# Optimization experiments

Hardware: AMD Instinct MI355X
Metric: run time of the kernel (lower is better)

## Reference

```python
import jax, jax.numpy as jnp
import numpy as np

CHEB_K = 3  # from init_kwargs


def setup_inputs() -> dict:
    key = jax.random.key(0)
    k1, k2, k3, k4 = jax.random.split(key, 4)
    B, N, C_IN, C_OUT, D = 32, 4096, 32, 64, 16
    x = jax.random.normal(k1, (B, N, C_IN), dtype=jnp.float32)
    node_embeddings = jax.random.normal(k2, (N, D), dtype=jnp.float32)
    laplacian_mx = jnp.zeros((N, N), dtype=jnp.float32)  # unused by forward
    weights_pool = jax.random.normal(k3, (D, CHEB_K, C_IN, C_OUT), dtype=jnp.float32) * 0.1
    bias_pool = jax.random.normal(k4, (D, C_OUT), dtype=jnp.float32) * 0.1
    return {
        'x': x,
        'node_embeddings': node_embeddings,
        'laplacian_mx': laplacian_mx,
        'weights_pool': weights_pool,
        'bias_pool': bias_pool,
    }


def reference(x, node_embeddings, laplacian_mx, weights_pool, bias_pool):
    N = node_embeddings.shape[0]
    # adaptive adjacency: softmax(relu(E E^T)) over rows
    supports = jax.nn.softmax(jax.nn.relu(node_embeddings @ node_embeddings.T), axis=1)
    # Chebyshev recursion T_0=I, T_1=A, T_k = 2A T_{k-1} - T_{k-2}
    support_set = [jnp.eye(N, dtype=x.dtype), supports]
    for _ in range(2, CHEB_K):
        support_set.append(2.0 * supports @ support_set[-1] - support_set[-2])
    supports_k = jnp.stack(support_set, axis=0)  # [K, N, N]
    # per-node generated weights/bias
    weights = jnp.einsum('nd,dkio->nkio', node_embeddings, weights_pool)  # [N,K,I,O]
    bias = node_embeddings @ bias_pool  # [N, O]
    # graph propagation: [K,N,N] x [B,N,I] -> [B,K,N,I] -> [B,N,K,I]
    x_g = jnp.einsum('knm,bmc->bknc', supports_k, x).transpose(0, 2, 1, 3)
    # per-node grouped GEMM
    out = jnp.einsum('bnki,nkio->bno', x_g, weights) + bias
    return out
```

## Files before the change

### kernel.cpp

```cpp
#include <hip/hip_runtime.h>
#include <hip/hip_bf16.h>

#define N_NODES 4096
#define BATCH   32
#define CIN     32
#define COUT    64
#define DEMB    16
#define NCOL    (BATCH * CIN)
#define KIO     (3 * CIN * COUT)
#define SPLITK  2

typedef __bf16 bf16x8 __attribute__((ext_vector_type(8)));
typedef float  floatx4 __attribute__((ext_vector_type(4)));

__device__ inline void load_lds16(const void* g, void* l) {
    __builtin_amdgcn_global_load_lds(
        (const __attribute__((address_space(1))) void*)g,
        (__attribute__((address_space(3))) void*)l, 16, 0, 0);
}

__global__ __launch_bounds__(256) void compute_U_kernel(
        const float* __restrict__ E, __hip_bfloat16* __restrict__ U,
        float* __restrict__ invRow) {
    const int n0   = blockIdx.x * 8;
    const int t    = threadIdx.x;
    const int lane = t & 63, wave = t >> 6;
    __shared__ float red[4][8];

    float en[8][DEMB];
#pragma unroll
    for (int r = 0; r < 8; ++r) {
        const float4* er = (const float4*)&E[(size_t)(n0 + r) * DEMB];
        const float4 a0 = er[0], a1 = er[1], a2 = er[2], a3 = er[3];
        en[r][ 0]=a0.x; en[r][ 1]=a0.y; en[r][ 2]=a0.z; en[r][ 3]=a0.w;
        en[r][ 4]=a1.x; en[r][ 5]=a1.y; en[r][ 6]=a1.z; en[r][ 7]=a1.w;
        en[r][ 8]=a2.x; en[r][ 9]=a2.y; en[r][10]=a2.z; en[r][11]=a2.w;
        en[r][12]=a3.x; en[r][13]=a3.y; en[r][14]=a3.z; en[r][15]=a3.w;
    }

    float sum[8] = {0.f, 0.f, 0.f, 0.f, 0.f, 0.f, 0.f, 0.f};

    for (int tile = 0; tile < 16; ++tile) {
        const int c = tile * 256 + t;
        const float4* em4 = (const float4*)&E[(size_t)c * DEMB];
        const float4 b0 = em4[0], b1 = em4[1], b2 = em4[2], b3 = em4[3];
        float em[DEMB];
        em[ 0]=b0.x; em[ 1]=b0.y; em[ 2]=b0.z; em[ 3]=b0.w;
        em[ 4]=b1.x; em[ 5]=b1.y; em[ 6]=b1.z; em[ 7]=b1.w;
        em[ 8]=b2.x; em[ 9]=b2.y; em[10]=b2.z; em[11]=b2.w;
        em[12]=b3.x; em[13]=b3.y; em[14]=b3.z; em[15]=b3.w;
#pragma unroll
        for (int r = 0; r < 8; ++r) {
            float dt = 0.f;
#pragma unroll
            for (int d = 0; d < DEMB; ++d) dt += en[r][d] * em[d];
            const float ev = __expf(fmaxf(dt, 0.f));
            sum[r] += ev;
            U[(size_t)(n0 + r) * N_NODES + c] = __float2bfloat16(ev);
        }
    }
#pragma unroll
    for (int r = 0; r < 8; ++r)
#pragma unroll
        for (int off = 32; off > 0; off >>= 1) sum[r] += __shfl_xor(sum[r], off);
    if (lane == 0)
#pragma unroll
        for (int r = 0; r < 8; ++r) red[wave][r] = sum[r];
    __syncthreads();
    if (t < 8)
        invRow[n0 + t] = 1.0f / (red[0][t] + red[1][t] + red[2][t] + red[3][t]);
}

__global__ __launch_bounds__(256) void transpose_kernel(
        const float* __restrict__ x,
        __hip_bfloat16* __restrict__ Xt, __hip_bfloat16* __restrict__ Bt) {
    const int m0 = blockIdx.x * 64;
    const int b  = blockIdx.y;
    const int t  = threadIdx.x;
    __shared__ float tile[64][33];
    {
        const int ml = t >> 2, cg = (t & 3) * 8;
        const float* src = &x[((size_t)b * N_NODES + (m0 + ml)) * CIN + cg];
        const float4 r0 = *(const float4*)src;
        const float4 r1 = *(const float4*)(src + 4);
        tile[ml][cg+0] = r0.x; tile[ml][cg+1] = r0.y; tile[ml][cg+2] = r0.z; tile[ml][cg+3] = r0.w;
        tile[ml][cg+4] = r1.x; tile[ml][cg+5] = r1.y; tile[ml][cg+6] = r1.z; tile[ml][cg+7] = r1.w;
    }
    __syncthreads();
    {
        const int ml = t >> 2, cg = (t & 3) * 8;
        __hip_bfloat16* dst = &Xt[(size_t)(m0 + ml) * NCOL + b * CIN + cg];
#pragma unroll
        for (int j = 0; j < 8; ++j) dst[j] = __float2bfloat16(tile[ml][cg + j]);
    }
    {
        const int c = t >> 3, mg = (t & 7) * 8;
        __hip_bfloat16* dst = &Bt[(size_t)(b * CIN + c) * N_NODES + m0 + mg];
#pragma unroll
        for (int j = 0; j < 8; ++j) dst[j] = __float2bfloat16(tile[mg + j][c]);
    }
}

__global__ __launch_bounds__(256) void gen_w_kernel(
        const float* __restrict__ E, const float* __restrict__ Wp,
        __hip_bfloat16* __restrict__ Wn) {
    const int c   = blockIdx.x >> 3;
    const int oo0 = (blockIdx.x & 7) * 8;
    const int nc  = blockIdx.y * 64;
    const int t   = threadIdx.x;
    const int kk  = t & 31;
    const int oo  = oo0 + (t >> 5);

    __shared__ float et[64][DEMB];
    ((float4*)et)[t] = ((const float4*)&E[(size_t)nc * DEMB])[t];
    __syncthreads();

    const int srccol = (c * 32 + kk) * 64 + oo;
    float w[DEMB];
#pragma unroll
    for (int d = 0; d < DEMB; ++d) w[d] = Wp[(size_t)d * KIO + srccol];

    const int dstoff = c * 2048 + (oo >> 4) * 512 + (oo & 15) * 32 + kk;
    for (int nl = 0; nl < 64; ++nl) {
        float acc = 0.0f;
#pragma unroll
        for (int d = 0; d < DEMB; ++d) acc += et[nl][d] * w[d];
        Wn[(size_t)(nc + nl) * KIO + dstoff] = __float2bfloat16(acc);
    }
}

#define GBM 256
#define GBN 128
#define GBK 64
#define NBUF 3

__global__ __launch_bounds__(512, 2) void gemm_splitk_kernel(
        const __hip_bfloat16* __restrict__ A,
        const __hip_bfloat16* __restrict__ Bt,
        __hip_bfloat16* __restrict__ P,
        int M, int NC, int K) {
    const int t    = threadIdx.x;
    const int row0 = blockIdx.x * GBM;
    const int col0 = blockIdx.y * GBN;
    const int z    = blockIdx.z;
    const int NT   = (K >> 6) / SPLITK;
    const int kb0  = z * NT * GBK;

    __shared__ alignas(16) __hip_bfloat16 As[NBUF][GBM * GBK];
    __shared__ alignas(16) __hip_bfloat16 Bs[NBUF][GBN * GBK];

    const int lane = t & 63, wave = t >> 6;
    const int l16 = lane & 15, quad = lane >> 4;
    const int wr = wave >> 1, wc = wave & 1;
    const int wrow = wr * 64, wcol = wc * 64;
    const int xr = l16 & 7;

    auto stageA = [&](int buf, int kb, int s) {
        const int gi = s * 512 + t;
        const int r  = gi >> 3;
        const int cg = (gi & 7) ^ (r & 7);
        load_lds16(&A[(size_t)(row0 + r) * K + kb + cg * 8], &As[buf][gi * 8]);
    };
    auto stageB = [&](int buf, int kb, int s) {
        const int gi = s * 512 + t;
        const int r  = gi >> 3;
        const int cg = (gi & 7) ^ (r & 7);
        load_lds16(&Bt[(size_t)(col0 + r) * K + kb + cg * 8], &Bs[buf][gi * 8]);
    };

    floatx4 acc[4][4] = {};

#pragma unroll
    for (int s = 0; s < 4; ++s) stageA(0, kb0, s);
#pragma unroll
    for (int s = 0; s < 2; ++s) stageB(0, kb0, s);
#pragma unroll
    for (int s = 0; s < 4; ++s) stageA(1, kb0 + GBK, s);
#pragma unroll
    for (int s = 0; s < 2; ++s) stageB(1, kb0 + GBK, s);
    asm volatile("s_waitcnt vmcnt(6)" ::: "memory");
    __builtin_amdgcn_s_barrier();
    __builtin_amdgcn_sched_barrier(0);

    int cur = 0;
    for (int tt = 0; tt < NT; ++tt) {
        const int  nb  = (cur + 2 >= NBUF) ? cur + 2 - NBUF : cur + 2;
        const int  kbn = kb0 + (tt + 2) * GBK;
        const bool pf  = (tt + 2 < NT);

        bf16x8 af0[4], bf0[4];
#pragma unroll
        for (int i = 0; i < 4; ++i)
            af0[i] = *(const bf16x8*)&As[cur][(wrow + i * 16 + l16) * GBK +
                                             ((quad ^ xr) * 8)];
#pragma unroll
        for (int j = 0; j < 4; ++j)
            bf0[j] = *(const bf16x8*)&Bs[cur][(wcol + j * 16 + l16) * GBK +
                                             ((quad ^ xr) * 8)];
        if (pf) { stageA(nb, kbn, 0); stageA(nb, kbn, 1); stageB(nb, kbn, 0); }
        __builtin_amdgcn_s_barrier();
        __builtin_amdgcn_s_setprio(1);
#pragma unroll
        for (int i = 0; i < 4; ++i)
#pragma unroll
            for (int j = 0; j < 4; ++j)
                acc[i][j] = __builtin_amdgcn_mfma_f32_16x16x32_bf16(
                                af0[i], bf0[j], acc[i][j], 0, 0, 0);
        __builtin_amdgcn_s_setprio(0);
        __builtin_amdgcn_s_barrier();

        bf16x8 af1[4], bf1[4];
#pragma unroll
        for (int i = 0; i < 4; ++i)
            af1[i] = *(const bf16x8*)&As[cur][(wrow + i * 16 + l16) * GBK +
                                             (((4 + quad) ^ xr) * 8)];
#pragma unroll
        for (int j = 0; j < 4; ++j)
            bf1[j] = *(const bf16x8*)&Bs[cur][(wcol + j * 16 + l16) * GBK +
                                             (((4 + quad) ^ xr) * 8)];
        if (pf) { stageA(nb, kbn, 2); stageA(nb, kbn, 3); stageB(nb, kbn, 1); }
        __builtin_amdgcn_s_barrier();
        __builtin_amdgcn_s_setprio(1);
#pragma unroll
        for (int i = 0; i < 4; ++i)
#pragma unroll
            for (int j = 0; j < 4; ++j)
                acc[i][j] = __builtin_amdgcn_mfma_f32_16x16x32_bf16(
                                af1[i], bf1[j], acc[i][j], 0, 0, 0);
        __builtin_amdgcn_s_setprio(0);
        if (pf) asm volatile("s_waitcnt vmcnt(6)" ::: "memory");
        else    asm volatile("s_waitcnt vmcnt(0)" ::: "memory");
        __builtin_amdgcn_s_barrier();
        __builtin_amdgcn_sched_barrier(0);

        cur = (cur + 1 == NBUF) ? 0 : cur + 1;
    }

    __hip_bfloat16* Pz = P + (size_t)z * M * NC;
#pragma unroll
    for (int i = 0; i < 4; ++i)
#pragma unroll
        for (int j = 0; j < 4; ++j)
#pragma unroll
            for (int r = 0; r < 4; ++r) {
                const int rg = row0 + wrow + i * 16 + quad * 4 + r;
                const int cg = col0 + wcol + j * 16 + l16;
                Pz[(size_t)rg * NC + cg] = __float2bfloat16(acc[i][j][r]);
            }
}

__global__ __launch_bounds__(256) void combine1_kernel(
        const __hip_bfloat16* __restrict__ P, const float* __restrict__ invRow,
        __hip_bfloat16* __restrict__ Y, __hip_bfloat16* __restrict__ Yt,
        int M, int NC) {
    const int c0 = blockIdx.x * 64, m0 = blockIdx.y * 64;
    const int t = threadIdx.x;
    __shared__ float tile[64][65];
    const size_t stride = (size_t)M * NC;
#pragma unroll
    for (int j = 0; j < 16; ++j) {
        const int lin = t + j * 256;
        const int r = lin >> 6, c = lin & 63;
        const size_t idx = (size_t)(m0 + r) * NC + c0 + c;
        float s = 0.f;
#pragma unroll
        for (int z = 0; z < SPLITK; ++z) s += __bfloat162float(P[idx + z * stride]);
        s *= invRow[m0 + r];
        tile[r][c] = s;
        Y[idx] = __float2bfloat16(s);
    }
    __syncthreads();
#pragma unroll
    for (int j = 0; j < 16; ++j) {
        const int lin = t + j * 256;
        const int c = lin >> 6, r = lin & 63;
        Yt[(size_t)(c0 + c) * M + m0 + r] = __float2bfloat16(tile[r][c]);
    }
}

__global__ __launch_bounds__(256) void combine2_kernel(
        const __hip_bfloat16* __restrict__ P, const float* __restrict__ invRow,
        const __hip_bfloat16* __restrict__ sub, __hip_bfloat16* __restrict__ Y2,
        int M, int NC) {
    const size_t stride = (size_t)M * NC;
    const size_t idx0 = (size_t)blockIdx.x * 4096 + threadIdx.x;
#pragma unroll
    for (int j = 0; j < 16; ++j) {
        const size_t idx = idx0 + (size_t)j * 256;
        float s = 0.f;
#pragma unroll
        for (int z = 0; z < SPLITK; ++z) s += __bfloat162float(P[idx + z * stride]);
        s *= invRow[idx >> 10];
        Y2[idx] = __float2bfloat16(2.0f * s - __bfloat162float(sub[idx]));
    }
}

__global__ __launch_bounds__(256) void final_kernel(
        const __hip_bfloat16* __restrict__ Xt, const __hip_bfloat16* __restrict__ Y1,
        const __hip_bfloat16* __restrict__ Y2, const __hip_bfloat16* __restrict__ Wn,
        const float* __restrict__ E, const float* __restrict__ bias_pool,
        float* __restrict__ out) {
    const int t    = threadIdx.x;
    const int lane = t & 63, wave = t >> 6;
    const int l16  = lane & 15, quad = lane >> 4;
    const int n    = blockIdx.x * 4 + wave;

    const __hip_bfloat16* srcs[3] = {Xt, Y1, Y2};
    const __hip_bfloat16* Wnode = Wn + (size_t)n * KIO;

    floatx4 acc[2][4] = {};

#pragma unroll
    for (int c = 0; c < 3; ++c) {
        bf16x8 af[2];
#pragma unroll
        for (int mt = 0; mt < 2; ++mt)
            af[mt] = *(const bf16x8*)&srcs[c][(size_t)n * NCOL +
                                              (mt * 16 + l16) * 32 + quad * 8];
#pragma unroll
        for (int ot = 0; ot < 4; ++ot) {
            const bf16x8 bfr = *(const bf16x8*)&Wnode[(size_t)c * 2048 +
                                                      ot * 512 + l16 * 32 + quad * 8];
#pragma unroll
            for (int mt = 0; mt < 2; ++mt)
                acc[mt][ot] = __builtin_amdgcn_mfma_f32_16x16x32_bf16(
                                  af[mt], bfr, acc[mt][ot], 0, 0, 0);
        }
    }

    float en[DEMB];
#pragma unroll
    for (int d = 0; d < DEMB; ++d) en[d] = E[(size_t)n * DEMB + d];
#pragma unroll
    for (int ot = 0; ot < 4; ++ot) {
        float bv = 0.f;
        const int o = ot * 16 + l16;
#pragma unroll
        for (int d = 0; d < DEMB; ++d) bv += en[d] * bias_pool[d * COUT + o];
#pragma unroll
        for (int mt = 0; mt < 2; ++mt)
#pragma unroll
            for (int r = 0; r < 4; ++r) {
                const int b = mt * 16 + quad * 4 + r;
                out[((size_t)b * N_NODES + n) * COUT + o] = acc[mt][ot][r] + bv;
            }
    }
}

extern "C" void kernel_launch(void* const* d_in, const int* in_sizes, int n_in,
                              void* d_out, int out_size, void* d_ws, size_t ws_size,
                              hipStream_t stream) {
    (void)in_sizes; (void)n_in; (void)out_size; (void)ws_size;
    const float* x  = (const float*)d_in[0];
    const float* E  = (const float*)d_in[1];
    const float* Wp = (const float*)d_in[3];
    const float* bp = (const float*)d_in[4];
    float* out = (float*)d_out;

    char* ws = (char*)d_ws;
    __hip_bfloat16* U   = (__hip_bfloat16*)(ws);
    __hip_bfloat16* Xt  = (__hip_bfloat16*)(ws + 33554432);
    __hip_bfloat16* Bt1 = (__hip_bfloat16*)(ws + 41943040);
    __hip_bfloat16* Y1  = (__hip_bfloat16*)(ws + 50331648);
    __hip_bfloat16* Y1t = (__hip_bfloat16*)(ws + 58720256);
    __hip_bfloat16* P   = (__hip_bfloat16*)(ws + 67108864);
    float*       invRow = (float*)(ws + 67108864 + 25165824);
    __hip_bfloat16* Wn  = (__hip_bfloat16*)(ws + 67108864);

    compute_U_kernel<<<N_NODES / 8, 256, 0, stream>>>(E, U, invRow);
    transpose_kernel<<<dim3(N_NODES / 64, BATCH), 256, 0, stream>>>(x, Xt, Bt1);
    gemm_splitk_kernel<<<dim3(N_NODES / GBM, NCOL / GBN, SPLITK), 512, 0, stream>>>(
        U, Bt1, P, N_NODES, NCOL, N_NODES);
    combine1_kernel<<<dim3(NCOL / 64, N_NODES / 64), 256, 0, stream>>>(
        P, invRow, Y1, Y1t, N_NODES, NCOL);
    gemm_splitk_kernel<<<dim3(N_NODES / GBM, NCOL / GBN, SPLITK), 512, 0, stream>>>(
        U, Y1t, P, N_NODES, NCOL, N_NODES);
    combine2_kernel<<<dim3(N_NODES * NCOL / 4096), 256, 0, stream>>>(
        P, invRow, Xt, Bt1, N_NODES, NCOL);
    gen_w_kernel<<<dim3(24, N_NODES / 64), 256, 0, stream>>>(E, Wp, Wn);
    final_kernel<<<N_NODES / 4, 256, 0, stream>>>(Xt, Y1, Bt1, Wn, E, bp, out);
}
```

Measured before the change: 270.2 us.

## Enlarge GEMM tile to 256x256 with half-K staged double buffering and split-K 4

Widens the split-K GEMM block tile from 256x128 to 256x256, so each wave now computes a 128x64 output region. The K tile is split into two 32-wide halves, staged with a new paired-row XOR swizzle into two LDS buffers instead of three. Split-K goes from 2 to 4 to keep enough blocks in flight, and the invRow workspace offset moves to fit the larger partial buffer. The aim is more reuse of each A and B tile per LDS read. The cost is a doubled accumulator register count, more partial-sum traffic for the combine kernels, and possible occupancy loss.

```diff
diff --git a/kernel.cpp b/kernel.cpp
--- a/kernel.cpp
+++ b/kernel.cpp
@@ -8,7 +8,7 @@
 #define DEMB    16
 #define NCOL    (BATCH * CIN)
 #define KIO     (3 * CIN * COUT)
-#define SPLITK  2
+#define SPLITK  4
 
 typedef __bf16 bf16x8 __attribute__((ext_vector_type(8)));
 typedef float  floatx4 __attribute__((ext_vector_type(4)));
@@ -130,9 +130,8 @@
 }
 
 #define GBM 256
-#define GBN 128
+#define GBN 256
 #define GBK 64
-#define NBUF 3
 
 __global__ __launch_bounds__(512, 2) void gemm_splitk_kernel(
         const __hip_bfloat16* __restrict__ A,
@@ -146,107 +145,157 @@
     const int NT   = (K >> 6) / SPLITK;
     const int kb0  = z * NT * GBK;
 
-    __shared__ alignas(16) __hip_bfloat16 As[NBUF][GBM * GBK];
-    __shared__ alignas(16) __hip_bfloat16 Bs[NBUF][GBN * GBK];
+    __shared__ alignas(16) __hip_bfloat16 As[2][16384];
+    __shared__ alignas(16) __hip_bfloat16 Bs[2][16384];
 
     const int lane = t & 63, wave = t >> 6;
     const int l16 = lane & 15, quad = lane >> 4;
-    const int wr = wave >> 1, wc = wave & 1;
-    const int wrow = wr * 64, wcol = wc * 64;
-    const int xr = l16 & 7;
-
-    auto stageA = [&](int buf, int kb, int s) {
-        const int gi = s * 512 + t;
-        const int r  = gi >> 3;
-        const int cg = (gi & 7) ^ (r & 7);
-        load_lds16(&A[(size_t)(row0 + r) * K + kb + cg * 8], &As[buf][gi * 8]);
+    const int wr = wave >> 2, wc = wave & 3;
+
+    const int R0 = wr * 128 + l16;
+    const int C0 = wc * 64 + l16;
+    const int u_par = (l16 & 1) * 4 + quad;
+    const int Aoff = (R0 >> 1) * 64 + ((u_par ^ ((R0 >> 1) & 7)) * 8);
+    const int Boff = (C0 >> 1) * 64 + ((u_par ^ ((C0 >> 1) & 7)) * 8);
+
+    auto stageA = [&](int buf, int kb, int kh, int s) {
+        const int L = s * 512 + t;
+        const int p = L >> 3, j = L & 7;
+        const int u = j ^ (p & 7);
+        const int rr = p * 2 + (u >> 2);
+        const int qq = u & 3;
+        load_lds16(&A[(size_t)(row0 + rr) * K + kb + kh * 32 + qq * 8],
+                   &As[buf][(size_t)(kh * 1024 + L) * 8]);
     };
-    auto stageB = [&](int buf, int kb, int s) {
-        const int gi = s * 512 + t;
-        const int r  = gi >> 3;
-        const int cg = (gi & 7) ^ (r & 7);
-        load_lds16(&Bt[(size_t)(col0 + r) * K + kb + cg * 8], &Bs[buf][gi * 8]);
+    auto stageB = [&](int buf, int kb, int kh, int s) {
+        const int L = s * 512 + t;
+        const int p = L >> 3, j = L & 7;
+        const int u = j ^ (p & 7);
+        const int rr = p * 2 + (u >> 2);
+        const int qq = u & 3;
+        load_lds16(&Bt[(size_t)(col0 + rr) * K + kb + kh * 32 + qq * 8],
+                   &Bs[buf][(size_t)(kh * 1024 + L) * 8]);
     };
 
-    floatx4 acc[4][4] = {};
-
-#pragma unroll
-    for (int s = 0; s < 4; ++s) stageA(0, kb0, s);
-#pragma unroll
-    for (int s = 0; s < 2; ++s) stageB(0, kb0, s);
-#pragma unroll
-    for (int s = 0; s < 4; ++s) stageA(1, kb0 + GBK, s);
-#pragma unroll
-    for (int s = 0; s < 2; ++s) stageB(1, kb0 + GBK, s);
-    asm volatile("s_waitcnt vmcnt(6)" ::: "memory");
+    floatx4 acc[8][4] = {};
+
+#pragma unroll
+    for (int s = 0; s < 2; ++s) stageA(0, kb0, 0, s);
+#pragma unroll
+    for (int s = 0; s < 2; ++s) stageB(0, kb0, 0, s);
+#pragma unroll
+    for (int s = 0; s < 2; ++s) stageA(0, kb0, 1, s);
+#pragma unroll
+    for (int s = 0; s < 2; ++s) stageB(0, kb0, 1, s);
+#pragma unroll
+    for (int s = 0; s < 2; ++s) stageA(1, kb0 + GBK, 0, s);
+#pragma unroll
+    for (int s = 0; s < 2; ++s) stageB(1, kb0 + GBK, 0, s);
+    asm volatile("s_waitcnt vmcnt(4)" ::: "memory");
     __builtin_amdgcn_s_barrier();
     __builtin_amdgcn_sched_barrier(0);
 
-    int cur = 0;
     for (int tt = 0; tt < NT; ++tt) {
-        const int  nb  = (cur + 2 >= NBUF) ? cur + 2 - NBUF : cur + 2;
-        const int  kbn = kb0 + (tt + 2) * GBK;
-        const bool pf  = (tt + 2 < NT);
-
-        bf16x8 af0[4], bf0[4];
-#pragma unroll
-        for (int i = 0; i < 4; ++i)
-            af0[i] = *(const bf16x8*)&As[cur][(wrow + i * 16 + l16) * GBK +
-                                             ((quad ^ xr) * 8)];
-#pragma unroll
-        for (int j = 0; j < 4; ++j)
-            bf0[j] = *(const bf16x8*)&Bs[cur][(wcol + j * 16 + l16) * GBK +
-                                             ((quad ^ xr) * 8)];
-        if (pf) { stageA(nb, kbn, 0); stageA(nb, kbn, 1); stageB(nb, kbn, 0); }
-        __builtin_amdgcn_s_barrier();
+        const int buf = tt & 1;
+        const int nb1 = (tt + 1) & 1;
+        const int nb2 = buf;
+        const int kb1 = kb0 + (tt + 1) * GBK;
+        const int kb2 = kb0 + (tt + 2) * GBK;
+        const bool g1 = (tt + 1 < NT), g2 = (tt + 2 < NT);
+
+        bf16x8 bfrag[4], afrag[4];
+
+#pragma unroll
+        for (int n = 0; n < 4; ++n)
+            bfrag[n] = *(const bf16x8*)&Bs[buf][n * 512 + Boff];
+#pragma unroll
+        for (int m = 0; m < 4; ++m)
+            afrag[m] = *(const bf16x8*)&As[buf][m * 512 + Aoff];
+        if (g1) { stageA(nb1, kb1, 1, 0); stageA(nb1, kb1, 1, 1); }
+        __builtin_amdgcn_s_barrier();
+        asm volatile("s_waitcnt lgkmcnt(0)" ::: "memory");
+        __builtin_amdgcn_sched_barrier(0);
         __builtin_amdgcn_s_setprio(1);
 #pragma unroll
-        for (int i = 0; i < 4; ++i)
-#pragma unroll
-            for (int j = 0; j < 4; ++j)
-                acc[i][j] = __builtin_amdgcn_mfma_f32_16x16x32_bf16(
-                                af0[i], bf0[j], acc[i][j], 0, 0, 0);
+        for (int m = 0; m < 4; ++m)
+#pragma unroll
+            for (int n = 0; n < 4; ++n)
+                acc[m][n] = __builtin_amdgcn_mfma_f32_16x16x32_bf16(
+                                afrag[m], bfrag[n], acc[m][n], 0, 0, 0);
         __builtin_amdgcn_s_setprio(0);
         __builtin_amdgcn_s_barrier();
 
-        bf16x8 af1[4], bf1[4];
-#pragma unroll
-        for (int i = 0; i < 4; ++i)
-            af1[i] = *(const bf16x8*)&As[cur][(wrow + i * 16 + l16) * GBK +
-                                             (((4 + quad) ^ xr) * 8)];
-#pragma unroll
-        for (int j = 0; j < 4; ++j)
-            bf1[j] = *(const bf16x8*)&Bs[cur][(wcol + j * 16 + l16) * GBK +
-                                             (((4 + quad) ^ xr) * 8)];
-        if (pf) { stageA(nb, kbn, 2); stageA(nb, kbn, 3); stageB(nb, kbn, 1); }
-        __builtin_amdgcn_s_barrier();
+#pragma unroll
+        for (int m = 0; m < 4; ++m)
+            afrag[m] = *(const bf16x8*)&As[buf][2048 + m * 512 + Aoff];
+        if (g1) { stageB(nb1, kb1, 1, 0); stageB(nb1, kb1, 1, 1); }
+        __builtin_amdgcn_s_barrier();
+        asm volatile("s_waitcnt lgkmcnt(0)" ::: "memory");
+        __builtin_amdgcn_sched_barrier(0);
         __builtin_amdgcn_s_setprio(1);
 #pragma unroll
-        for (int i = 0; i < 4; ++i)
-#pragma unroll
-            for (int j = 0; j < 4; ++j)
-                acc[i][j] = __builtin_amdgcn_mfma_f32_16x16x32_bf16(
-                                af1[i], bf1[j], acc[i][j], 0, 0, 0);
+        for (int m = 0; m < 4; ++m)
+#pragma unroll
+            for (int n = 0; n < 4; ++n)
+                acc[4 + m][n] = __builtin_amdgcn_mfma_f32_16x16x32_bf16(
+                                    afrag[m], bfrag[n], acc[4 + m][n], 0, 0, 0);
         __builtin_amdgcn_s_setprio(0);
-        if (pf) asm volatile("s_waitcnt vmcnt(6)" ::: "memory");
-        else    asm volatile("s_waitcnt vmcnt(0)" ::: "memory");
-        __builtin_amdgcn_s_barrier();
+        __builtin_amdgcn_s_barrier();
+
+#pragma unroll
+        for (int n = 0; n < 4; ++n)
+            bfrag[n] = *(const bf16x8*)&Bs[buf][8192 + n * 512 + Boff];
+#pragma unroll
+        for (int m = 0; m < 4; ++m)
+            afrag[m] = *(const bf16x8*)&As[buf][8192 + m * 512 + Aoff];
+        if (g2) { stageA(nb2, kb2, 0, 0); stageA(nb2, kb2, 0, 1); }
+        __builtin_amdgcn_s_barrier();
+        asm volatile("s_waitcnt lgkmcnt(0)" ::: "memory");
         __builtin_amdgcn_sched_barrier(0);
-
-        cur = (cur + 1 == NBUF) ? 0 : cur + 1;
+        __builtin_amdgcn_s_setprio(1);
+#pragma unroll
+        for (int m = 0; m < 4; ++m)
+#pragma unroll
+            for (int n = 0; n < 4; ++n)
+                acc[m][n] = __builtin_amdgcn_mfma_f32_16x16x32_bf16(
+                                afrag[m], bfrag[n], acc[m][n], 0, 0, 0);
+        __builtin_amdgcn_s_setprio(0);
+        __builtin_amdgcn_s_barrier();
+
+#pragma unroll
+        for (int m = 0; m < 4; ++m)
+            afrag[m] = *(const bf16x8*)&As[buf][8192 + 2048 + m * 512 + Aoff];
+        if (g2) { stageB(nb2, kb2, 0, 0); stageB(nb2, kb2, 0, 1); }
+        __builtin_amdgcn_s_barrier();
+        asm volatile("s_waitcnt lgkmcnt(0)" ::: "memory");
+        __builtin_amdgcn_sched_barrier(0);
+        __builtin_amdgcn_s_setprio(1);
+#pragma unroll
+        for (int m = 0; m < 4; ++m)
+#pragma unroll
+            for (int n = 0; n < 4; ++n)
+                acc[4 + m][n] = __builtin_amdgcn_mfma_f32_16x16x32_bf16(
+                                    afrag[m], bfrag[n], acc[4 + m][n], 0, 0, 0);
+        __builtin_amdgcn_s_setprio(0);
+        if (tt < NT - 2) asm volatile("s_waitcnt vmcnt(4)" ::: "memory");
+        else             asm volatile("s_waitcnt vmcnt(0)" ::: "memory");
+        __builtin_amdgcn_s_barrier();
+        __builtin_amdgcn_sched_barrier(0);
     }
 
     __hip_bfloat16* Pz = P + (size_t)z * M * NC;
 #pragma unroll
-    for (int i = 0; i < 4; ++i)
-#pragma unroll
-        for (int j = 0; j < 4; ++j)
-#pragma unroll
-            for (int r = 0; r < 4; ++r) {
-                const int rg = row0 + wrow + i * 16 + quad * 4 + r;
-                const int cg = col0 + wcol + j * 16 + l16;
-                Pz[(size_t)rg * NC + cg] = __float2bfloat16(acc[i][j][r]);
-            }
+    for (int mq = 0; mq < 2; ++mq)
+#pragma unroll
+        for (int m = 0; m < 4; ++m)
+#pragma unroll
+            for (int n = 0; n < 4; ++n)
+#pragma unroll
+                for (int r = 0; r < 4; ++r) {
+                    const int rg = row0 + wr * 128 + mq * 64 + m * 16 + quad * 4 + r;
+                    const int cg = col0 + wc * 64 + n * 16 + l16;
+                    Pz[(size_t)rg * NC + cg] = __float2bfloat16(acc[mq * 4 + m][n][r]);
+                }
 }
 
 __global__ __launch_bounds__(256) void combine1_kernel(
@@ -364,7 +413,7 @@
     __hip_bfloat16* Y1  = (__hip_bfloat16*)(ws + 50331648);
     __hip_bfloat16* Y1t = (__hip_bfloat16*)(ws + 58720256);
     __hip_bfloat16* P   = (__hip_bfloat16*)(ws + 67108864);
-    float*       invRow = (float*)(ws + 67108864 + 25165824);
+    float*       invRow = (float*)(ws + 100663296);
     __hip_bfloat16* Wn  = (__hip_bfloat16*)(ws + 67108864);
 
     compute_U_kernel<<<N_NODES / 8, 256, 0, stream>>>(E, U, invRow);
```

After: 279.6 us. 1.03x slower.
